# Kernel tuning notes

Measured on AMD Instinct MI355X. Metric: run time of the kernel, lower is better.

The kernel has to match this reference:

```python
import jax, jax.numpy as jnp
import numpy as np

B = 128          # batch size
N_KG = 500       # KG vertices
N = N_KG + 2     # + sensor node + zero target node
D = 1024         # embed_dim (hard-coded in forward)
H = 256          # gnn_hidden
E = 4000         # edges
EPS = 1e-5


def setup_inputs() -> dict:
    key = jax.random.key(0)
    ks = jax.random.split(key, 8)
    return {
        "sensor_batch": jax.random.normal(ks[0], (B, D), jnp.float32),
        "base_vertices": jax.random.normal(ks[1], (N_KG, D), jnp.float32),
        "edge_index": jax.random.randint(ks[2], (2, E), 0, N, jnp.int64),
        "W1": jax.random.normal(ks[3], (D, H), jnp.float32) * (1.0 / np.sqrt(D)),
        "b1": jnp.zeros((H,), jnp.float32),
        "gamma1": jnp.ones((H,), jnp.float32),
        "beta1": jnp.zeros((H,), jnp.float32),
        "W2": jax.random.normal(ks[4], (H, H), jnp.float32) * (1.0 / np.sqrt(H)),
        "b2": jnp.zeros((H,), jnp.float32),
        "gamma2": jnp.ones((H,), jnp.float32),
        "beta2": jnp.zeros((H,), jnp.float32),
        "W3": jax.random.normal(ks[5], (H, H), jnp.float32) * (1.0 / np.sqrt(H)),
        "b3": jnp.zeros((H,), jnp.float32),
        "gamma3": jnp.ones((H,), jnp.float32),
        "beta3": jnp.zeros((H,), jnp.float32),
    }


def _gcn_norm(edge_index):
    # add self loops, symmetric normalization D^{-1/2} A D^{-1/2}
    loops = jnp.arange(N, dtype=edge_index.dtype)
    src = jnp.concatenate([edge_index[0], loops])
    dst = jnp.concatenate([edge_index[1], loops])
    deg = jnp.zeros((N,), jnp.float32).at[dst].add(1.0)
    dinv = jnp.where(deg > 0, jax.lax.rsqrt(deg), 0.0)
    norm = dinv[src] * dinv[dst]   # [E+N]
    return src, dst, norm


def _gcn_conv(x, W, b, src, dst, norm):
    # x: [B, N, F_in] -> [B, N, F_out]
    h = jnp.einsum('bnf,fh->bnh', x, W)
    msg = h[:, src, :] * norm[None, :, None]            # gather + scale
    out = jnp.zeros_like(h).at[:, dst, :].add(msg)      # scatter-add
    return out + b


def _bn_elu(x, gamma, beta):
    # BatchNorm1d over flattened (B*N, H) in training mode, then ELU
    Bn, Nn, Hh = x.shape
    xf = x.reshape(Bn * Nn, Hh)
    mean = jnp.mean(xf, axis=0)
    var = jnp.mean(jnp.square(xf - mean), axis=0)  # biased, as in torch BN fwd
    y = (xf - mean) * jax.lax.rsqrt(var + EPS) * gamma + beta
    return jax.nn.elu(y).reshape(Bn, Nn, Hh)


def reference(sensor_batch, base_vertices, edge_index,
              W1, b1, gamma1, beta1,
              W2, b2, gamma2, beta2,
              W3, b3, gamma3, beta3):
    Bn = sensor_batch.shape[0]
    # x = [base_vertices; sensor_input; zeros] per batch element -> [B, N, D]
    base = jnp.broadcast_to(base_vertices[None], (Bn, N_KG, D))
    zeros = jnp.zeros((Bn, 1, D), sensor_batch.dtype)
    x = jnp.concatenate([base, sensor_batch[:, None, :], zeros], axis=1)

    src, dst, norm = _gcn_norm(edge_index)
    x = _bn_elu(_gcn_conv(x, W1, b1, src, dst, norm), gamma1, beta1)
    x = _bn_elu(_gcn_conv(x, W2, b2, src, dst, norm), gamma2, beta2)
    x = _bn_elu(_gcn_conv(x, W3, b3, src, dst, norm), gamma3, beta3)
    return x
```

## Files before the change

### kernel.cpp

```cpp
#include <hip/hip_runtime.h>
#include <cstdint>
#include <cstddef>

#define NNODES 502
#define NKG    500
#define NPAD   512
#define NEDGE  4000
#define NET    4502
#define BB     128
#define DD     1024
#define HH     256
#define MROWS  (BB*NNODES)
#define MT     65536
#define MCAT   628
#define EPITCH 136

typedef short short8 __attribute__((ext_vector_type(8)));
typedef float f32x4  __attribute__((ext_vector_type(4)));

__device__ __forceinline__ unsigned short f2bf(float f) {
  union { float f; unsigned int u; } v; v.f = f;
  unsigned int r = v.u + 0x7fffu + ((v.u >> 16) & 1u);
  return (unsigned short)(r >> 16);
}

__device__ __forceinline__ float bf2f(unsigned short u) {
  union { unsigned int u; float f; } v; v.u = ((unsigned int)u) << 16;
  return v.f;
}

__device__ __forceinline__ float elu(float y) {
  return (y > 0.f) ? y : (__expf(y) - 1.f);
}

__device__ __forceinline__ void stage16(const void* g, void* l) {
  __builtin_amdgcn_global_load_lds((__attribute__((address_space(1))) void*)g,
                                   (__attribute__((address_space(3))) void*)l, 16, 0, 0);
}

__device__ __forceinline__ void mfma16(f32x4& c, short8 a, short8 b) {
  asm volatile("v_mfma_f32_16x16x32_bf16 %0, %1, %2, %0" : "+v"(c) : "v"(a), "v"(b));
}

__device__ inline void get_edge(const int* __restrict__ e, int i, int i64mode,
                                int& src, int& dst) {
  if (i < NEDGE) {
    if (i64mode) { src = e[2*i]; dst = e[2*NEDGE + 2*i]; }
    else         { src = e[i];   dst = e[NEDGE + i]; }
  } else {
    src = dst = i - NEDGE;
  }
  src = min(max(src, 0), NNODES-1);
  dst = min(max(dst, 0), NNODES-1);
}

__device__ __forceinline__ int detect_mode(const int* __restrict__ e) {
  __shared__ int sflag;
  if (threadIdx.x == 0) sflag = 0;
  __syncthreads();
  if (e[2*threadIdx.x + 1] != 0) atomicOr(&sflag, 1);
  __syncthreads();
  return sflag == 0;
}

__global__ void deg_kernel(const int* __restrict__ e, int* __restrict__ deg) {
  int i64 = detect_mode(e);
  int i = blockIdx.x*256 + threadIdx.x;
  if (i >= NET) return;
  int src, dst; get_edge(e, i, i64, src, dst);
  atomicAdd(&deg[dst], 1);
}

__global__ void scan_kernel(const int* __restrict__ deg, float* __restrict__ dinv,
                            int* __restrict__ rp, int* __restrict__ cursor) {
  __shared__ int s[512];
  int t = threadIdx.x;
  int cnt = (t < NNODES) ? deg[t] : 0;
  s[t] = cnt;
  if (t < NNODES) dinv[t] = rsqrtf((float)cnt);
  __syncthreads();
  for (int off = 1; off < 512; off <<= 1) {
    int v = (t >= off) ? s[t-off] : 0;
    __syncthreads();
    s[t] += v;
    __syncthreads();
  }
  if (t == 0) rp[0] = 0;
  if (t < NNODES) { rp[t+1] = s[t]; cursor[t] = s[t] - cnt; }
}

__global__ void fillsdf_kernel(const int* __restrict__ e, const float* __restrict__ dinv,
                               int* __restrict__ cursor, int* __restrict__ colA,
                               float* __restrict__ valA, float* __restrict__ Sdf) {
  int i64 = detect_mode(e);
  int i = blockIdx.x*256 + threadIdx.x;
  if (i >= NET) return;
  int src, dst; get_edge(e, i, i64, src, dst);
  float v = dinv[src] * dinv[dst];
  int pos = atomicAdd(&cursor[dst], 1);
  colA[pos] = src;
  valA[pos] = v;
  atomicAdd(&Sdf[dst*NPAD + src], v);
}

__global__ void sdcvt_kernel(const float* __restrict__ Sdf, unsigned short* __restrict__ Sd) {
  int i = blockIdx.x*256 + threadIdx.x;
  Sd[i] = f2bf(Sdf[i]);
}

__global__ __launch_bounds__(256) void prep_kernel(
    const float* __restrict__ W1, const float* __restrict__ W2, const float* __restrict__ W3,
    const float* __restrict__ base, const float* __restrict__ sensor,
    unsigned short* __restrict__ Wt1, unsigned short* __restrict__ Wt2,
    unsigned short* __restrict__ Wt3, unsigned short* __restrict__ Xp1,
    float* __restrict__ hcatz) {
  int bid = blockIdx.x, tid = threadIdx.x;
  if (bid < 512) {
    const float* W = (bid & 256) ? W3 : W2;
    unsigned short* Wt = (bid & 256) ? Wt3 : Wt2;
    int n = bid & 255;
    Wt[n*HH + tid] = f2bf(W[(size_t)tid*HH + n]);
  } else if (bid < 768) {
    int n = bid - 512;
    for (int k = tid; k < DD; k += 256)
      Wt1[n*DD + k] = f2bf(W1[(size_t)k*HH + n]);
  } else if (bid < 1408) {
    int i = (bid - 768)*256 + tid;
    int r = i >> 8, c = (i & 255) * 4;
    float4 v = make_float4(0.f, 0.f, 0.f, 0.f);
    if (r < NKG) v = *(const float4*)&base[(size_t)r*DD + c];
    else if (r < MCAT) v = *(const float4*)&sensor[(size_t)(r-NKG)*DD + c];
    union { unsigned short u[4]; uint2 d; } p;
    p.u[0]=f2bf(v.x); p.u[1]=f2bf(v.y); p.u[2]=f2bf(v.z); p.u[3]=f2bf(v.w);
    *(uint2*)&Xp1[(size_t)r*DD + c] = p.d;
  } else {
    hcatz[(bid - 1408)*256 + tid] = 0.f;
  }
}

__global__ __launch_bounds__(256) void gemm1m_kernel(
    const unsigned short* __restrict__ Ag,
    const unsigned short* __restrict__ Bg,
    float* __restrict__ C) {
  __shared__ unsigned short As[128*32];
  __shared__ unsigned short Bs[128*32];
  int tid = threadIdx.x;
  int wave = tid >> 6, lane = tid & 63;
  int l15 = lane & 15, quad = lane >> 4;
  int wm = (wave & 1) * 64, wn = (wave >> 1) * 64;
  int row0 = blockIdx.y * 128, col0 = blockIdx.x * 128;
  int kbase = blockIdx.z * 256;
  f32x4 acc[4][4] = {};
  for (int k0 = kbase; k0 < kbase + 256; k0 += 32) {
#pragma unroll
    for (int q = 0; q < 2; ++q) {
      int c = wave*128 + q*64 + lane;
      stage16(Ag + (size_t)(row0 + (c>>2))*DD + k0 + (c&3)*8, As + c*8);
      stage16(Bg + (size_t)(col0 + (c>>2))*DD + k0 + (c&3)*8, Bs + c*8);
    }
    __syncthreads();
    short8 af[4], bfv[4];
#pragma unroll
    for (int i = 0; i < 4; ++i) {
      af[i]  = *(const short8*)(As + (wm + i*16 + l15)*32 + quad*8);
      bfv[i] = *(const short8*)(Bs + (wn + i*16 + l15)*32 + quad*8);
    }
#pragma unroll
    for (int mi = 0; mi < 4; ++mi)
#pragma unroll
      for (int ni = 0; ni < 4; ++ni)
        mfma16(acc[mi][ni], af[mi], bfv[ni]);
    __syncthreads();
  }
  asm volatile("s_nop 7\n\ts_nop 7" ::);
#pragma unroll
  for (int ni = 0; ni < 4; ++ni) {
    int n = col0 + wn + ni*16 + l15;
#pragma unroll
    for (int mi = 0; mi < 4; ++mi) {
      int m = row0 + wm + mi*16 + quad*4;
#pragma unroll
      for (int r = 0; r < 4; ++r)
        if (m + r < MCAT) atomicAdd(&C[(size_t)(m+r)*HH + n], acc[mi][ni][r]);
    }
  }
}

__global__ void ac_kernel(const int* __restrict__ rp, const int* __restrict__ colA,
                          const float* __restrict__ valA, const float* __restrict__ hcat,
                          float* __restrict__ Abuf, float* __restrict__ cbuf) {
  int n = blockIdx.x, h = threadIdx.x;
  int s = rp[n], e = rp[n+1];
  float acc = 0.f, cacc = 0.f;
  for (int t = s; t < e; ++t) {
    int cl = colA[t]; float v = valA[t];
    if (cl < NKG) acc += v * hcat[cl*HH + h];
    else if (cl == NKG) cacc += v;
  }
  Abuf[n*HH + h] = acc;
  if (h == 0) cbuf[n] = cacc;
}

__global__ __launch_bounds__(256) void bn1n_kernel(
    const float* __restrict__ Abuf, const float* __restrict__ cbuf,
    const float* __restrict__ hcat,
    float* __restrict__ sA1, float* __restrict__ sAA1, float* __restrict__ sAc1,
    float* __restrict__ scp, float* __restrict__ ssA, float* __restrict__ sssA) {
  int bid = blockIdx.x, h = threadIdx.x;
  if (bid < 32) {
    int n0 = bid*16, n1 = min(n0+16, NNODES);
    float sA = 0, sAA = 0, sAc = 0, sc = 0, scc = 0;
    for (int n = n0; n < n1; ++n) {
      float a = Abuf[n*HH + h]; float cn = cbuf[n];
      sA += a; sAA += a*a; sAc += a*cn; sc += cn; scc += cn*cn;
    }
    atomicAdd(&sA1[h], sA); atomicAdd(&sAA1[h], sAA); atomicAdd(&sAc1[h], sAc);
    if (h == 0) { atomicAdd(&scp[0], sc); atomicAdd(&scp[1], scc); }
  } else {
    int b0 = (bid-32)*16;
    float ss = 0, sss = 0;
    for (int b = b0; b < b0+16; ++b) {
      float v = hcat[(size_t)(NKG + b)*HH + h]; ss += v; sss += v*v;
    }
    atomicAdd(&ssA[h], ss); atomicAdd(&sssA[h], sss);
  }
}

__global__ void fin1_kernel(const float* __restrict__ sA1, const float* __restrict__ sAA1,
                            const float* __restrict__ sAc1, const float* __restrict__ scp,
                            const float* __restrict__ ssA, const float* __restrict__ sssA,
                            const float* __restrict__ gamma, const float* __restrict__ beta,
                            float* __restrict__ scale, float* __restrict__ shift) {
  int h = threadIdx.x;
  float sA = sA1[h], sAA = sAA1[h], sAc = sAc1[h];
  float sc = scp[0], scc = scp[1];
  float ss = ssA[h], sss = sssA[h];
  const float cnt = (float)MROWS;
  float mean = ((float)BB * sA + sc*ss) / cnt;
  float msq  = ((float)BB * sAA + 2.f*sAc*ss + scc*sss) / cnt;
  float var  = msq - mean*mean;
  float scl  = gamma[h] * rsqrtf(var + 1e-5f);
  scale[h] = scl; shift[h] = beta[h] - mean*scl;
}

__global__ __launch_bounds__(256) void x2_kernel(
    const float* __restrict__ Abuf, const float* __restrict__ cbuf,
    const float* __restrict__ hcat, const float* __restrict__ scale,
    const float* __restrict__ shift, unsigned short* __restrict__ Xb) {
  int idx = blockIdx.x*256 + threadIdx.x;
  int row = idx >> 6, h0 = (idx & 63)*4;
  int b = row >> 9, n = row & (NPAD-1);
  union { unsigned short u[4]; uint2 d; } p;
  p.d = make_uint2(0,0);
  if (n < NNODES) {
    float4 a  = *(const float4*)(Abuf + n*HH + h0);
    float4 s  = *(const float4*)(hcat + (size_t)(NKG + b)*HH + h0);
    float4 sc = *(const float4*)(scale + h0);
    float4 sh = *(const float4*)(shift + h0);
    float cn = cbuf[n];
    p.u[0] = f2bf(elu((a.x + cn*s.x)*sc.x + sh.x));
    p.u[1] = f2bf(elu((a.y + cn*s.y)*sc.y + sh.y));
    p.u[2] = f2bf(elu((a.z + cn*s.z)*sc.z + sh.z));
    p.u[3] = f2bf(elu((a.w + cn*s.w)*sc.w + sh.w));
  }
  *(uint2*)(Xb + (size_t)row*HH + h0) = p.d;
}

template<int FBN>
__global__ __launch_bounds__(256) void gemmT2_kernel(
    const unsigned short* __restrict__ Ag,
    const unsigned short* __restrict__ Bg,
    const float* __restrict__ sums, const float* __restrict__ ssqs,
    const float* __restrict__ gamma, const float* __restrict__ beta,
    unsigned short* __restrict__ Tt) {
  __shared__ __align__(16) unsigned short smem[25600];
  unsigned short* As = smem;
  unsigned short* Bs = smem + 8192;
  float* sclL = (float*)(smem + 24576);
  float* shfL = sclL + 256;
  int tid = threadIdx.x;
  int wave = tid >> 6, lane = tid & 63;
  int l15 = lane & 15, quad = lane >> 4;
  int wm = (wave & 1) * 64;
  int wnh = wave >> 1;
  int row0 = blockIdx.x * 128;
  if (FBN) {
    float mean = sums[tid] * (1.f/(float)MROWS);
    float var  = ssqs[tid] * (1.f/(float)MROWS) - mean*mean;
    float s = gamma[tid] * rsqrtf(var + 1e-5f);
    sclL[tid] = s; shfL[tid] = beta[tid] - mean*s;
    __syncthreads();
  }
  f32x4 acc[4][8] = {};
  for (int k0 = 0; k0 < HH; k0 += 64) {
#pragma unroll
    for (int q = 0; q < 8; ++q) {
      int c = q*256 + tid;
      int kb = c >> 10, rr = (c >> 2) & 255, j = c & 3;
      stage16(Bg + (size_t)rr*HH + k0 + kb*32 + j*8, Bs + c*8);
    }
#pragma unroll
    for (int q = 0; q < 4; ++q) {
      int c = q*256 + tid;
      int half = c >> 9, rr = (c >> 2) & 127, j = c & 3;
      int kk = k0 + half*32 + j*8;
      if (FBN) {
        union { unsigned short u[8]; uint4 d; } va, pa;
        va.d = *(const uint4*)(Ag + (size_t)(row0 + rr)*HH + kk);
#pragma unroll
        for (int t = 0; t < 8; ++t)
          pa.u[t] = f2bf(elu(bf2f(va.u[t])*sclL[kk+t] + shfL[kk+t]));
        *(uint4*)(As + c*8) = pa.d;
      } else {
        stage16(Ag + (size_t)(row0 + rr)*HH + kk, As + c*8);
      }
    }
    __syncthreads();
#pragma unroll
    for (int kb = 0; kb < 2; ++kb) {
      short8 af[4], bfv[8];
#pragma unroll
      for (int i = 0; i < 4; ++i)
        af[i] = *(const short8*)(As + kb*4096 + (wm + i*16 + l15)*32 + quad*8);
#pragma unroll
      for (int i = 0; i < 8; ++i)
        bfv[i] = *(const short8*)(Bs + kb*8192 + (wnh*128 + i*16 + l15)*32 + quad*8);
#pragma unroll
      for (int mi = 0; mi < 4; ++mi)
#pragma unroll
        for (int ni = 0; ni < 8; ++ni)
          mfma16(acc[mi][ni], af[mi], bfv[ni]);
    }
    __syncthreads();
  }
  asm volatile("s_nop 7\n\ts_nop 7" ::);
  int moff = (tid & 15)*8;
#pragma unroll
  for (int nh = 0; nh < 2; ++nh) {
    if (wnh == nh) {
#pragma unroll
      for (int ni = 0; ni < 8; ++ni) {
        int nl = ni*16 + l15;
#pragma unroll
        for (int mi = 0; mi < 4; ++mi) {
          int ml = wm + mi*16 + quad*4;
#pragma unroll
          for (int r = 0; r < 4; ++r)
            smem[nl*EPITCH + ml + r] = f2bf(acc[mi][ni][r]);
        }
      }
    }
    __syncthreads();
#pragma unroll
    for (int j = 0; j < 8; ++j) {
      int nr = (tid >> 4) + j*16;
      uint4 d = *(const uint4*)(smem + nr*EPITCH + moff);
      *(uint4*)(Tt + (size_t)(nh*128 + nr)*MT + row0 + moff) = d;
    }
    __syncthreads();
  }
}

__global__ __launch_bounds__(256) void gemmS_kernel(
    const unsigned short* __restrict__ Sd,
    const unsigned short* __restrict__ Tt,
    unsigned short* __restrict__ Xbo,
    float* __restrict__ sums, float* __restrict__ ssqs) {
  __shared__ __align__(16) unsigned short smem[128*EPITCH];
  unsigned short* As = smem;
  unsigned short* Bs = smem + 8192;
  int tid = threadIdx.x;
  int wave = tid >> 6, lane = tid & 63;
  int l15 = lane & 15, quad = lane >> 4;
  int wm = (wave & 1) * 64, wn = (wave >> 1) * 64;
  int id = blockIdx.x;
  int xcd = id & 7;
  int w = id >> 3;
  int y = w & 3;
  int g = (w >> 2) * 8 + xcd;
  int x = g >> 7;
  int b = g & 127;
  int row0 = y * 128, col0 = x * 128;
  f32x4 acc[4][4] = {};
  for (int k0 = 0; k0 < NPAD; k0 += 64) {
#pragma unroll
    for (int q = 0; q < 4; ++q) {
      int c = q*256 + wave*64 + lane;
      int half = c >> 9, rr = (c >> 2) & 127, j = c & 3;
      stage16(Sd + (size_t)(row0 + rr)*NPAD + k0 + half*32 + j*8, As + c*8);
      stage16(Tt + (size_t)(col0 + rr)*MT + b*NPAD + k0 + half*32 + j*8, Bs + c*8);
    }
    __syncthreads();
#pragma unroll
    for (int kb = 0; kb < 2; ++kb) {
      short8 af[4], bfv[4];
#pragma unroll
      for (int i = 0; i < 4; ++i) {
        af[i]  = *(const short8*)(As + kb*4096 + (wm + i*16 + l15)*32 + quad*8);
        bfv[i] = *(const short8*)(Bs + kb*4096 + (wn + i*16 + l15)*32 + quad*8);
      }
#pragma unroll
      for (int mi = 0; mi < 4; ++mi)
#pragma unroll
        for (int ni = 0; ni < 4; ++ni)
          mfma16(acc[mi][ni], af[mi], bfv[ni]);
    }
    __syncthreads();
  }
  asm volatile("s_nop 7\n\ts_nop 7" ::);
  float ps[4] = {0,0,0,0}, pq[4] = {0,0,0,0};
#pragma unroll
  for (int ni = 0; ni < 4; ++ni)
#pragma unroll
    for (int mi = 0; mi < 4; ++mi)
#pragma unroll
      for (int r = 0; r < 4; ++r) {
        float v = acc[mi][ni][r];
        ps[ni] += v; pq[ni] += v*v;
      }
#pragma unroll
  for (int mi = 0; mi < 4; ++mi) {
    int ml = wm + mi*16 + quad*4;
#pragma unroll
    for (int ni = 0; ni < 4; ++ni) {
      int nl = wn + ni*16 + l15;
#pragma unroll
      for (int r = 0; r < 4; ++r)
        smem[(ml + r)*EPITCH + nl] = f2bf(acc[mi][ni][r]);
    }
  }
  __syncthreads();
  unsigned short* Xrow = Xbo + (size_t)b*NPAD*HH;
  int noff = (tid & 15)*8;
#pragma unroll
  for (int j = 0; j < 8; ++j) {
    int rr = (tid >> 4) + j*16;
    int node = row0 + rr;
    if (node < NNODES) {
      uint4 d = *(const uint4*)(smem + rr*EPITCH + noff);
      *(uint4*)(Xrow + (size_t)node*HH + col0 + noff) = d;
    }
  }
  __syncthreads();
  float* red = (float*)smem;
  red[tid] = 0.f;
  __syncthreads();
#pragma unroll
  for (int ni = 0; ni < 4; ++ni) {
    int cl = wn + ni*16 + l15;
    atomicAdd(&red[cl], ps[ni]);
    atomicAdd(&red[128+cl], pq[ni]);
  }
  __syncthreads();
  if (tid < 128) atomicAdd(&sums[col0+tid], red[tid]);
  else atomicAdd(&ssqs[col0+tid-128], red[tid]);
}

__global__ void finalize_kernel(const float* __restrict__ sums, const float* __restrict__ ssqs,
                                const float* __restrict__ gamma, const float* __restrict__ beta,
                                float* __restrict__ scale, float* __restrict__ shift) {
  int h = threadIdx.x;
  const float cnt = (float)MROWS;
  float mean = sums[h] / cnt;
  float var  = ssqs[h] / cnt - mean*mean;
  float scl  = gamma[h] * rsqrtf(var + 1e-5f);
  scale[h] = scl; shift[h] = beta[h] - mean*scl;
}

__global__ __launch_bounds__(256) void bnout_kernel(
    const unsigned short* __restrict__ Xb, const float* __restrict__ scale,
    const float* __restrict__ shift, float* __restrict__ O) {
  int idx = blockIdx.x*256 + threadIdx.x;
  int row = idx >> 6, h0 = (idx & 63)*4;
  int b = row >> 9, n = row & (NPAD-1);
  if (n >= NNODES) return;
  union { unsigned short u[4]; uint2 d; } v;
  v.d = *(const uint2*)(Xb + (size_t)row*HH + h0);
  float4 sc = *(const float4*)(scale + h0);
  float4 sh = *(const float4*)(shift + h0);
  float4 o;
  o.x = elu(bf2f(v.u[0])*sc.x + sh.x);
  o.y = elu(bf2f(v.u[1])*sc.y + sh.y);
  o.z = elu(bf2f(v.u[2])*sc.z + sh.z);
  o.w = elu(bf2f(v.u[3])*sc.w + sh.w);
  *(float4*)(O + ((size_t)(b*NNODES + n)*HH + h0)) = o;
}

extern "C" void kernel_launch(void* const* d_in, const int* in_sizes, int n_in,
                              void* d_out, int out_size, void* d_ws, size_t ws_size,
                              hipStream_t stream) {
  const float* sensor = (const float*)d_in[0];
  const float* base   = (const float*)d_in[1];
  const int*   eidx   = (const int*)d_in[2];
  const float* W1 = (const float*)d_in[3];
  const float* g1 = (const float*)d_in[5];
  const float* be1= (const float*)d_in[6];
  const float* W2 = (const float*)d_in[7];
  const float* g2 = (const float*)d_in[9];
  const float* be2= (const float*)d_in[10];
  const float* W3 = (const float*)d_in[11];
  const float* g3 = (const float*)d_in[13];
  const float* be3= (const float*)d_in[14];

  char* ws = (char*)d_ws;
  int*   deg    = (int*)(ws + 0);
  float* sum2   = (float*)(ws + 2048);
  float* ssq2   = (float*)(ws + 3072);
  float* sum3   = (float*)(ws + 4096);
  float* ssq3   = (float*)(ws + 5120);
  float* cbuf   = (float*)(ws + 6144);
  int*   cursor = (int*)(ws + 8192);
  float* sA1    = (float*)(ws + 10496);
  float* sAA1   = (float*)(ws + 11520);
  float* sAc1   = (float*)(ws + 12544);
  float* scp    = (float*)(ws + 13568);
  float* ssA    = (float*)(ws + 13824);
  float* sssA   = (float*)(ws + 14848);
  float* dinv   = (float*)(ws + 16384);
  int*   rp     = (int*)(ws + 18432);
  int*   colA   = (int*)(ws + 20480);
  float* valA   = (float*)(ws + 40960);
  float* scale1 = (float*)(ws + 61440);
  float* shift1 = (float*)(ws + 62464);
  float* scale3 = (float*)(ws + 65536);
  float* shift3 = (float*)(ws + 66560);
  float* Abuf   = (float*)(ws + 67584);
  float* hcat   = (float*)(ws + 581632);
  unsigned short* Wt2 = (unsigned short*)(ws + 1224704);
  unsigned short* Wt3 = (unsigned short*)(ws + 1355776);
  unsigned short* Sd  = (unsigned short*)(ws + 1486848);
  unsigned short* Xb  = (unsigned short*)(ws + 2011136);
  unsigned short* Tt  = (unsigned short*)(ws + 35565568UL);
  unsigned short* Xp1 = (unsigned short*)(ws + 35565568UL);
  unsigned short* Wt1 = (unsigned short*)(ws + 35565568UL + 1310720);
  float* out = (float*)d_out;
  float* Sdf = (float*)d_out;

  hipMemsetAsync(ws, 0, 16384, stream);
  hipMemsetAsync(d_out, 0, NPAD*NPAD*4, stream);
  deg_kernel<<<(NET+255)/256, 256, 0, stream>>>(eidx, deg);
  scan_kernel<<<1, 512, 0, stream>>>(deg, dinv, rp, cursor);
  fillsdf_kernel<<<(NET+255)/256, 256, 0, stream>>>(eidx, dinv, cursor, colA, valA, Sdf);
  sdcvt_kernel<<<(NPAD*NPAD)/256, 256, 0, stream>>>(Sdf, Sd);
  prep_kernel<<<2036, 256, 0, stream>>>(W1, W2, W3, base, sensor, Wt1, Wt2, Wt3, Xp1, hcat);

  gemm1m_kernel<<<dim3(2, 5, 4), 256, 0, stream>>>(Xp1, Wt1, hcat);
  ac_kernel<<<NNODES, 256, 0, stream>>>(rp, colA, valA, hcat, Abuf, cbuf);
  bn1n_kernel<<<40, 256, 0, stream>>>(Abuf, cbuf, hcat, sA1, sAA1, sAc1, scp, ssA, sssA);
  fin1_kernel<<<1, 256, 0, stream>>>(sA1, sAA1, sAc1, scp, ssA, sssA, g1, be1, scale1, shift1);
  x2_kernel<<<(MT*64)/256, 256, 0, stream>>>(Abuf, cbuf, hcat, scale1, shift1, Xb);

  gemmT2_kernel<0><<<MT/128, 256, 0, stream>>>(Xb, Wt2, sum2, ssq2, g2, be2, Tt);
  gemmS_kernel<<<1024, 256, 0, stream>>>(Sd, Tt, Xb, sum2, ssq2);
  gemmT2_kernel<1><<<MT/128, 256, 0, stream>>>(Xb, Wt3, sum2, ssq2, g2, be2, Tt);
  gemmS_kernel<<<1024, 256, 0, stream>>>(Sd, Tt, Xb, sum3, ssq3);
  finalize_kernel<<<1, 256, 0, stream>>>(sum3, ssq3, g3, be3, scale3, shift3);
  bnout_kernel<<<(MT*64)/256, 256, 0, stream>>>(Xb, scale3, shift3, out);
}
```

Measured before the change: 314.1 us.

## Double-buffer LDS in both GEMM kernels to overlap loads with MFMA

Both the feature-transform GEMM and the aggregation GEMM switch from single-buffered 64-wide K steps to double-buffered 32-wide K steps. The next tile's global-to-LDS loads are issued before the current tile's MFMAs, with explicit vmcnt waits and raw barriers. In the BN-fused path the next A tile is loaded into registers and normalized/ELU'd after the MFMAs. The aim is to hide global memory latency behind compute, at the cost of more barriers per K and hand-tuned waitcnt counts that rely on stage16 being an async LDS load.

Result: no change. 312.1 us (-0.7%).

```diff
diff --git a/kernel.cpp b/kernel.cpp
--- a/kernel.cpp
+++ b/kernel.cpp
@@ -273,11 +273,10 @@
     const float* __restrict__ sums, const float* __restrict__ ssqs,
     const float* __restrict__ gamma, const float* __restrict__ beta,
     unsigned short* __restrict__ Tt) {
-  __shared__ __align__(16) unsigned short smem[25600];
+  __shared__ __align__(16) unsigned short smem[24576];
+  __shared__ float sclL[256], shfL[256];
   unsigned short* As = smem;
   unsigned short* Bs = smem + 8192;
-  float* sclL = (float*)(smem + 24576);
-  float* shfL = sclL + 256;
   int tid = threadIdx.x;
   int wave = tid >> 6, lane = tid & 63;
   int l15 = lane & 15, quad = lane >> 4;
@@ -291,47 +290,84 @@
     sclL[tid] = s; shfL[tid] = beta[tid] - mean*s;
     __syncthreads();
   }
+  int c0 = tid, c1 = 256 + tid;
+  int ar0 = c0 >> 2, ao0 = (c0 & 3) * 8;
+  int ar1 = c1 >> 2, ao1 = (c1 & 3) * 8;
+  const unsigned short* Arow0 = Ag + (size_t)(row0 + ar0)*HH + ao0;
+  const unsigned short* Arow1 = Ag + (size_t)(row0 + ar1)*HH + ao1;
+
   f32x4 acc[4][8] = {};
-  for (int k0 = 0; k0 < HH; k0 += 64) {
-#pragma unroll
-    for (int q = 0; q < 8; ++q) {
-      int c = q*256 + tid;
-      int kb = c >> 10, rr = (c >> 2) & 255, j = c & 3;
-      stage16(Bg + (size_t)rr*HH + k0 + kb*32 + j*8, Bs + c*8);
-    }
-#pragma unroll
-    for (int q = 0; q < 4; ++q) {
-      int c = q*256 + tid;
-      int half = c >> 9, rr = (c >> 2) & 127, j = c & 3;
-      int kk = k0 + half*32 + j*8;
+  uint4 rn0, rn1;
+  if (FBN) {
+    uint4 p0 = *(const uint4*)(Arow0);
+    uint4 p1 = *(const uint4*)(Arow1);
+    union { unsigned short u[8]; uint4 d; } va, pa;
+    va.d = p0;
+#pragma unroll
+    for (int s = 0; s < 8; ++s) pa.u[s] = f2bf(elu(bf2f(va.u[s])*sclL[ao0+s] + shfL[ao0+s]));
+    *(uint4*)(As + c0*8) = pa.d;
+    va.d = p1;
+#pragma unroll
+    for (int s = 0; s < 8; ++s) pa.u[s] = f2bf(elu(bf2f(va.u[s])*sclL[ao1+s] + shfL[ao1+s]));
+    *(uint4*)(As + c1*8) = pa.d;
+    asm volatile("s_waitcnt lgkmcnt(0)" ::: "memory");
+  } else {
+    stage16(Arow0, As + c0*8);
+    stage16(Arow1, As + c1*8);
+  }
+#pragma unroll
+  for (int q = 0; q < 4; ++q) {
+    int c = q*256 + tid; int rr = c >> 2, jj = (c & 3)*8;
+    stage16(Bg + (size_t)rr*HH + jj, Bs + c*8);
+  }
+  for (int t = 0; t < 8; ++t) {
+    int cur = t & 1;
+    int kn = (t+1) * 32;
+    if (t < 7) {
       if (FBN) {
-        union { unsigned short u[8]; uint4 d; } va, pa;
-        va.d = *(const uint4*)(Ag + (size_t)(row0 + rr)*HH + kk);
-#pragma unroll
-        for (int t = 0; t < 8; ++t)
-          pa.u[t] = f2bf(elu(bf2f(va.u[t])*sclL[kk+t] + shfL[kk+t]));
-        *(uint4*)(As + c*8) = pa.d;
+        rn0 = *(const uint4*)(Arow0 + kn);
+        rn1 = *(const uint4*)(Arow1 + kn);
       } else {
-        stage16(Ag + (size_t)(row0 + rr)*HH + kk, As + c*8);
+        stage16(Arow0 + kn, As + (cur^1)*4096 + c0*8);
+        stage16(Arow1 + kn, As + (cur^1)*4096 + c1*8);
       }
-    }
-    __syncthreads();
-#pragma unroll
-    for (int kb = 0; kb < 2; ++kb) {
-      short8 af[4], bfv[8];
-#pragma unroll
-      for (int i = 0; i < 4; ++i)
-        af[i] = *(const short8*)(As + kb*4096 + (wm + i*16 + l15)*32 + quad*8);
-#pragma unroll
-      for (int i = 0; i < 8; ++i)
-        bfv[i] = *(const short8*)(Bs + kb*8192 + (wnh*128 + i*16 + l15)*32 + quad*8);
-#pragma unroll
-      for (int mi = 0; mi < 4; ++mi)
-#pragma unroll
-        for (int ni = 0; ni < 8; ++ni)
-          mfma16(acc[mi][ni], af[mi], bfv[ni]);
-    }
-    __syncthreads();
+#pragma unroll
+      for (int q = 0; q < 4; ++q) {
+        int c = q*256 + tid; int rr = c >> 2, jj = (c & 3)*8;
+        stage16(Bg + (size_t)rr*HH + kn + jj, Bs + (cur^1)*8192 + c*8);
+      }
+      asm volatile("s_waitcnt vmcnt(6)" ::: "memory");
+    } else {
+      asm volatile("s_waitcnt vmcnt(0)" ::: "memory");
+    }
+    __builtin_amdgcn_s_barrier();
+    __builtin_amdgcn_sched_barrier(0);
+    short8 af[4], bfv[8];
+#pragma unroll
+    for (int i = 0; i < 4; ++i)
+      af[i] = *(const short8*)(As + cur*4096 + (wm + i*16 + l15)*32 + quad*8);
+#pragma unroll
+    for (int i = 0; i < 8; ++i)
+      bfv[i] = *(const short8*)(Bs + cur*8192 + (wnh*128 + i*16 + l15)*32 + quad*8);
+#pragma unroll
+    for (int mi = 0; mi < 4; ++mi)
+#pragma unroll
+      for (int ni = 0; ni < 8; ++ni)
+        mfma16(acc[mi][ni], af[mi], bfv[ni]);
+    if (FBN && t < 7) {
+      union { unsigned short u[8]; uint4 d; } va, pa;
+      va.d = rn0;
+#pragma unroll
+      for (int s = 0; s < 8; ++s) pa.u[s] = f2bf(elu(bf2f(va.u[s])*sclL[kn+ao0+s] + shfL[kn+ao0+s]));
+      *(uint4*)(As + (cur^1)*4096 + c0*8) = pa.d;
+      va.d = rn1;
+#pragma unroll
+      for (int s = 0; s < 8; ++s) pa.u[s] = f2bf(elu(bf2f(va.u[s])*sclL[kn+ao1+s] + shfL[kn+ao1+s]));
+      *(uint4*)(As + (cur^1)*4096 + c1*8) = pa.d;
+      asm volatile("s_waitcnt lgkmcnt(0)" ::: "memory");
+    }
+    __builtin_amdgcn_sched_barrier(0);
+    __builtin_amdgcn_s_barrier();
   }
   asm volatile("s_nop 7\n\ts_nop 7" ::);
   int moff = (tid & 15)*8;
@@ -381,31 +417,45 @@
   int x = g >> 7;
   int b = g & 127;
   int row0 = y * 128, col0 = x * 128;
+  const unsigned short* Abase = Sd + (size_t)row0*NPAD;
+  const unsigned short* Bbase = Tt + (size_t)col0*MT + (size_t)b*NPAD;
+  int c0 = tid, c1 = 256 + tid;
+  int r0s = c0 >> 2, o0 = (c0 & 3) * 8;
+  int r1s = c1 >> 2, o1 = (c1 & 3) * 8;
+
   f32x4 acc[4][4] = {};
-  for (int k0 = 0; k0 < NPAD; k0 += 64) {
-#pragma unroll
-    for (int q = 0; q < 4; ++q) {
-      int c = q*256 + wave*64 + lane;
-      int half = c >> 9, rr = (c >> 2) & 127, j = c & 3;
-      stage16(Sd + (size_t)(row0 + rr)*NPAD + k0 + half*32 + j*8, As + c*8);
-      stage16(Tt + (size_t)(col0 + rr)*MT + b*NPAD + k0 + half*32 + j*8, Bs + c*8);
-    }
-    __syncthreads();
-#pragma unroll
-    for (int kb = 0; kb < 2; ++kb) {
-      short8 af[4], bfv[4];
-#pragma unroll
-      for (int i = 0; i < 4; ++i) {
-        af[i]  = *(const short8*)(As + kb*4096 + (wm + i*16 + l15)*32 + quad*8);
-        bfv[i] = *(const short8*)(Bs + kb*4096 + (wn + i*16 + l15)*32 + quad*8);
-      }
-#pragma unroll
-      for (int mi = 0; mi < 4; ++mi)
-#pragma unroll
-        for (int ni = 0; ni < 4; ++ni)
-          mfma16(acc[mi][ni], af[mi], bfv[ni]);
-    }
-    __syncthreads();
+  stage16(Abase + (size_t)r0s*NPAD + o0, As + c0*8);
+  stage16(Abase + (size_t)r1s*NPAD + o1, As + c1*8);
+  stage16(Bbase + (size_t)r0s*MT + o0, Bs + c0*8);
+  stage16(Bbase + (size_t)r1s*MT + o1, Bs + c1*8);
+  for (int t = 0; t < 16; ++t) {
+    int cur = t & 1;
+    if (t < 15) {
+      int kn = (t+1)*32;
+      int nb = (cur^1)*4096;
+      stage16(Abase + (size_t)r0s*NPAD + kn + o0, As + nb + c0*8);
+      stage16(Abase + (size_t)r1s*NPAD + kn + o1, As + nb + c1*8);
+      stage16(Bbase + (size_t)r0s*MT + kn + o0, Bs + nb + c0*8);
+      stage16(Bbase + (size_t)r1s*MT + kn + o1, Bs + nb + c1*8);
+      asm volatile("s_waitcnt vmcnt(4)" ::: "memory");
+    } else {
+      asm volatile("s_waitcnt vmcnt(0)" ::: "memory");
+    }
+    __builtin_amdgcn_s_barrier();
+    __builtin_amdgcn_sched_barrier(0);
+    short8 af[4], bfv[4];
+#pragma unroll
+    for (int i = 0; i < 4; ++i) {
+      af[i]  = *(const short8*)(As + cur*4096 + (wm + i*16 + l15)*32 + quad*8);
+      bfv[i] = *(const short8*)(Bs + cur*4096 + (wn + i*16 + l15)*32 + quad*8);
+    }
+#pragma unroll
+    for (int mi = 0; mi < 4; ++mi)
+#pragma unroll
+      for (int ni = 0; ni < 4; ++ni)
+        mfma16(acc[mi][ni], af[mi], bfv[ni]);
+    __builtin_amdgcn_sched_barrier(0);
+    __builtin_amdgcn_s_barrier();
   }
   asm volatile("s_nop 7\n\ts_nop 7" ::);
   float ps[4] = {0,0,0,0}, pq[4] = {0,0,0,0};
```

## Double-buffer the aggregation GEMM K-loop with async global-to-LDS prefetch

Applied to the files above, without the earlier changes.

Restructures the aggregation kernel's K loop from 64-wide single-buffered steps into 32-wide steps over two LDS buffers. The next tile's loads are issued before computing the current one, and a partial vmcnt wait lets the loads overlap the MFMA work. Per-thread address math is hoisted out of the loop. This depends on stage16 being an asynchronous direct-to-LDS load counted by vmcnt, and the loop now runs twice as many barrier pairs.

Result: no change. 314.6 us (+0.1%).

```diff
diff --git a/kernel.cpp b/kernel.cpp
--- a/kernel.cpp
+++ b/kernel.cpp
@@ -381,31 +381,45 @@
   int x = g >> 7;
   int b = g & 127;
   int row0 = y * 128, col0 = x * 128;
+  const unsigned short* Abase = Sd + (size_t)row0*NPAD;
+  const unsigned short* Bbase = Tt + (size_t)col0*MT + (size_t)b*NPAD;
+  int c0 = tid, c1 = 256 + tid;
+  int r0s = c0 >> 2, o0 = (c0 & 3) * 8;
+  int r1s = c1 >> 2, o1 = (c1 & 3) * 8;
+
   f32x4 acc[4][4] = {};
-  for (int k0 = 0; k0 < NPAD; k0 += 64) {
-#pragma unroll
-    for (int q = 0; q < 4; ++q) {
-      int c = q*256 + wave*64 + lane;
-      int half = c >> 9, rr = (c >> 2) & 127, j = c & 3;
-      stage16(Sd + (size_t)(row0 + rr)*NPAD + k0 + half*32 + j*8, As + c*8);
-      stage16(Tt + (size_t)(col0 + rr)*MT + b*NPAD + k0 + half*32 + j*8, Bs + c*8);
-    }
-    __syncthreads();
-#pragma unroll
-    for (int kb = 0; kb < 2; ++kb) {
-      short8 af[4], bfv[4];
-#pragma unroll
-      for (int i = 0; i < 4; ++i) {
-        af[i]  = *(const short8*)(As + kb*4096 + (wm + i*16 + l15)*32 + quad*8);
-        bfv[i] = *(const short8*)(Bs + kb*4096 + (wn + i*16 + l15)*32 + quad*8);
-      }
-#pragma unroll
-      for (int mi = 0; mi < 4; ++mi)
-#pragma unroll
-        for (int ni = 0; ni < 4; ++ni)
-          mfma16(acc[mi][ni], af[mi], bfv[ni]);
-    }
-    __syncthreads();
+  stage16(Abase + (size_t)r0s*NPAD + o0, As + c0*8);
+  stage16(Abase + (size_t)r1s*NPAD + o1, As + c1*8);
+  stage16(Bbase + (size_t)r0s*MT + o0, Bs + c0*8);
+  stage16(Bbase + (size_t)r1s*MT + o1, Bs + c1*8);
+  for (int t = 0; t < 16; ++t) {
+    int cur = t & 1;
+    if (t < 15) {
+      int kn = (t+1)*32;
+      int nb = (cur^1)*4096;
+      stage16(Abase + (size_t)r0s*NPAD + kn + o0, As + nb + c0*8);
+      stage16(Abase + (size_t)r1s*NPAD + kn + o1, As + nb + c1*8);
+      stage16(Bbase + (size_t)r0s*MT + kn + o0, Bs + nb + c0*8);
+      stage16(Bbase + (size_t)r1s*MT + kn + o1, Bs + nb + c1*8);
+      asm volatile("s_waitcnt vmcnt(4)" ::: "memory");
+    } else {
+      asm volatile("s_waitcnt vmcnt(0)" ::: "memory");
+    }
+    __builtin_amdgcn_s_barrier();
+    __builtin_amdgcn_sched_barrier(0);
+    short8 af[4], bfv[4];
+#pragma unroll
+    for (int i = 0; i < 4; ++i) {
+      af[i]  = *(const short8*)(As + cur*4096 + (wm + i*16 + l15)*32 + quad*8);
+      bfv[i] = *(const short8*)(Bs + cur*4096 + (wn + i*16 + l15)*32 + quad*8);
+    }
+#pragma unroll
+    for (int mi = 0; mi < 4; ++mi)
+#pragma unroll
+      for (int ni = 0; ni < 4; ++ni)
+        mfma16(acc[mi][ni], af[mi], bfv[ni]);
+    __builtin_amdgcn_sched_barrier(0);
+    __builtin_amdgcn_s_barrier();
   }
   asm volatile("s_nop 7\n\ts_nop 7" ::);
   float ps[4] = {0,0,0,0}, pq[4] = {0,0,0,0};
```

## Process two batches per block in gemmS with triple-buffered async staging

Applied to the files above, without the earlier changes.

The aggregation GEMM now gives each block two batch elements, so the tile of the normalized adjacency matrix is loaded once and reused for both. Grid size is halved. The K loop switches from 64-wide steps with two syncthreads each to 32-wide steps over a three-stage shared-memory ring, using explicit vmcnt waits and barriers so global loads overlap the MFMA work. This doubles the accumulator registers and raises LDS use, which may lower occupancy.

Result: faster. 294.4 us (-6.3%).

```diff
diff --git a/kernel.cpp b/kernel.cpp
--- a/kernel.cpp
+++ b/kernel.cpp
@@ -361,14 +361,14 @@
   }
 }
 
-__global__ __launch_bounds__(256) void gemmS_kernel(
+__global__ __launch_bounds__(256) void gemmS2_kernel(
     const unsigned short* __restrict__ Sd,
     const unsigned short* __restrict__ Tt,
     unsigned short* __restrict__ Xbo,
     float* __restrict__ sums, float* __restrict__ ssqs) {
-  __shared__ __align__(16) unsigned short smem[128*EPITCH];
+  __shared__ __align__(16) unsigned short smem[36864];
   unsigned short* As = smem;
-  unsigned short* Bs = smem + 8192;
+  unsigned short* Bs = smem + 12288;
   int tid = threadIdx.x;
   int wave = tid >> 6, lane = tid & 63;
   int l15 = lane & 15, quad = lane >> 4;
@@ -378,70 +378,100 @@
   int w = id >> 3;
   int y = w & 3;
   int g = (w >> 2) * 8 + xcd;
-  int x = g >> 7;
-  int b = g & 127;
+  int x = g >> 6;
+  int b = (g & 63) * 2;
   int row0 = y * 128, col0 = x * 128;
-  f32x4 acc[4][4] = {};
-  for (int k0 = 0; k0 < NPAD; k0 += 64) {
+  const unsigned short* Abase = Sd + (size_t)row0*NPAD;
+  const unsigned short* Bbase = Tt + (size_t)col0*MT + (size_t)b*NPAD;
+  int c0 = tid, c1 = 256 + tid;
+  int r0 = c0 >> 2, o0 = (c0 & 3) * 8;
+  int r1 = c1 >> 2, o1 = (c1 & 3) * 8;
+
+  f32x4 acc[2][4][4] = {};
+  auto STAGE = [&](int kn, int buf) {
+    stage16(Abase + (size_t)r0*NPAD + kn + o0, As + buf*4096 + c0*8);
+    stage16(Abase + (size_t)r1*NPAD + kn + o1, As + buf*4096 + c1*8);
 #pragma unroll
     for (int q = 0; q < 4; ++q) {
-      int c = q*256 + wave*64 + lane;
-      int half = c >> 9, rr = (c >> 2) & 127, j = c & 3;
-      stage16(Sd + (size_t)(row0 + rr)*NPAD + k0 + half*32 + j*8, As + c*8);
-      stage16(Tt + (size_t)(col0 + rr)*MT + b*NPAD + k0 + half*32 + j*8, Bs + c*8);
-    }
-    __syncthreads();
-#pragma unroll
-    for (int kb = 0; kb < 2; ++kb) {
-      short8 af[4], bfv[4];
-#pragma unroll
-      for (int i = 0; i < 4; ++i) {
-        af[i]  = *(const short8*)(As + kb*4096 + (wm + i*16 + l15)*32 + quad*8);
-        bfv[i] = *(const short8*)(Bs + kb*4096 + (wn + i*16 + l15)*32 + quad*8);
-      }
+      int c = q*256 + tid;
+      int bb = c >> 9, cc = c & 511;
+      int rr = cc >> 2, j = (cc & 3)*8;
+      stage16(Bbase + (size_t)rr*MT + bb*NPAD + kn + j, Bs + buf*8192 + c*8);
+    }
+  };
+  STAGE(0, 0);
+  STAGE(32, 1);
+  for (int t = 0; t < 16; ++t) {
+    int cur = t % 3;
+    if (t < 14) {
+      STAGE((t+2)*32, (t+2) % 3);
+      asm volatile("s_waitcnt vmcnt(12)" ::: "memory");
+    } else if (t == 14) {
+      asm volatile("s_waitcnt vmcnt(6)" ::: "memory");
+    } else {
+      asm volatile("s_waitcnt vmcnt(0)" ::: "memory");
+    }
+    __builtin_amdgcn_s_barrier();
+    __builtin_amdgcn_sched_barrier(0);
+    short8 af[4], bfv[2][4];
+#pragma unroll
+    for (int i = 0; i < 4; ++i)
+      af[i] = *(const short8*)(As + cur*4096 + (wm + i*16 + l15)*32 + quad*8);
+#pragma unroll
+    for (int bb = 0; bb < 2; ++bb)
+#pragma unroll
+      for (int i = 0; i < 4; ++i)
+        bfv[bb][i] = *(const short8*)(Bs + cur*8192 + bb*4096 + (wn + i*16 + l15)*32 + quad*8);
+#pragma unroll
+    for (int bb = 0; bb < 2; ++bb)
 #pragma unroll
       for (int mi = 0; mi < 4; ++mi)
 #pragma unroll
         for (int ni = 0; ni < 4; ++ni)
-          mfma16(acc[mi][ni], af[mi], bfv[ni]);
-    }
-    __syncthreads();
+          mfma16(acc[bb][mi][ni], af[mi], bfv[bb][ni]);
+    __builtin_amdgcn_sched_barrier(0);
+    __builtin_amdgcn_s_barrier();
   }
   asm volatile("s_nop 7\n\ts_nop 7" ::);
   float ps[4] = {0,0,0,0}, pq[4] = {0,0,0,0};
 #pragma unroll
-  for (int ni = 0; ni < 4; ++ni)
-#pragma unroll
-    for (int mi = 0; mi < 4; ++mi)
-#pragma unroll
-      for (int r = 0; r < 4; ++r) {
-        float v = acc[mi][ni][r];
-        ps[ni] += v; pq[ni] += v*v;
+  for (int bb = 0; bb < 2; ++bb)
+#pragma unroll
+    for (int ni = 0; ni < 4; ++ni)
+#pragma unroll
+      for (int mi = 0; mi < 4; ++mi)
+#pragma unroll
+        for (int r = 0; r < 4; ++r) {
+          float v = acc[bb][mi][ni][r];
+          ps[ni] += v; pq[ni] += v*v;
+        }
+  int noff = (tid & 15)*8;
+#pragma unroll
+  for (int bb = 0; bb < 2; ++bb) {
+#pragma unroll
+    for (int mi = 0; mi < 4; ++mi) {
+      int ml = wm + mi*16 + quad*4;
+#pragma unroll
+      for (int ni = 0; ni < 4; ++ni) {
+        int nl = wn + ni*16 + l15;
+#pragma unroll
+        for (int r = 0; r < 4; ++r)
+          smem[(ml + r)*EPITCH + nl] = f2bf(acc[bb][mi][ni][r]);
       }
-#pragma unroll
-  for (int mi = 0; mi < 4; ++mi) {
-    int ml = wm + mi*16 + quad*4;
-#pragma unroll
-    for (int ni = 0; ni < 4; ++ni) {
-      int nl = wn + ni*16 + l15;
-#pragma unroll
-      for (int r = 0; r < 4; ++r)
-        smem[(ml + r)*EPITCH + nl] = f2bf(acc[mi][ni][r]);
-    }
-  }
-  __syncthreads();
-  unsigned short* Xrow = Xbo + (size_t)b*NPAD*HH;
-  int noff = (tid & 15)*8;
-#pragma unroll
-  for (int j = 0; j < 8; ++j) {
-    int rr = (tid >> 4) + j*16;
-    int node = row0 + rr;
-    if (node < NNODES) {
-      uint4 d = *(const uint4*)(smem + rr*EPITCH + noff);
-      *(uint4*)(Xrow + (size_t)node*HH + col0 + noff) = d;
-    }
-  }
-  __syncthreads();
+    }
+    __syncthreads();
+    unsigned short* Xrow = Xbo + (size_t)(b + bb)*NPAD*HH;
+#pragma unroll
+    for (int j = 0; j < 8; ++j) {
+      int rr = (tid >> 4) + j*16;
+      int node = row0 + rr;
+      if (node < NNODES) {
+        uint4 d = *(const uint4*)(smem + rr*EPITCH + noff);
+        *(uint4*)(Xrow + (size_t)node*HH + col0 + noff) = d;
+      }
+    }
+    __syncthreads();
+  }
   float* red = (float*)smem;
   red[tid] = 0.f;
   __syncthreads();
@@ -551,9 +581,9 @@
   x2_kernel<<<(MT*64)/256, 256, 0, stream>>>(Abuf, cbuf, hcat, scale1, shift1, Xb);
 
   gemmT2_kernel<0><<<MT/128, 256, 0, stream>>>(Xb, Wt2, sum2, ssq2, g2, be2, Tt);
-  gemmS_kernel<<<1024, 256, 0, stream>>>(Sd, Tt, Xb, sum2, ssq2);
+  gemmS2_kernel<<<512, 256, 0, stream>>>(Sd, Tt, Xb, sum2, ssq2);
   gemmT2_kernel<1><<<MT/128, 256, 0, stream>>>(Xb, Wt3, sum2, ssq2, g2, be2, Tt);
-  gemmS_kernel<<<1024, 256, 0, stream>>>(Sd, Tt, Xb, sum3, ssq3);
+  gemmS2_kernel<<<512, 256, 0, stream>>>(Sd, Tt, Xb, sum3, ssq3);
   finalize_kernel<<<1, 256, 0, stream>>>(sum3, ssq3, g3, be3, scale3, shift3);
   bnout_kernel<<<(MT*64)/256, 256, 0, stream>>>(Xb, scale3, shift3, out);
 }
```
